# Optimization experiments

Measured on AMD Instinct MI355X. Metric: run time of the kernel, lower is better.

The kernel has to match this reference:

```python
import jax, jax.numpy as jnp
import numpy as np
import math


def get_alibi_slopes(n_heads: int) -> np.ndarray:
    # Bloom-style ALiBi slopes.
    cp2 = 2 ** math.floor(math.log2(n_heads))
    base = 2.0 ** (-(2.0 ** -(math.log2(cp2) - 3)))
    slopes = base ** np.arange(1, cp2 + 1, dtype=np.float32)
    if cp2 != n_heads:
        extra_base = 2.0 ** (-(2.0 ** -(math.log2(2 * cp2) - 3)))
        extra = extra_base ** np.arange(1, 2 * (n_heads - cp2) + 1, 2, dtype=np.float32)
        slopes = np.concatenate([slopes, extra])
    return slopes.astype(np.float32)


def setup_inputs() -> dict:
    key = jax.random.key(0)
    k1, k2, k3 = jax.random.split(key, 3)
    B, S, D, H = 2, 2048, 2048, 16
    T = B * S
    return {
        "hidden_states": jax.random.normal(k1, (T, D), dtype=jnp.float32) * 0.02,
        "qkv_weight": jax.random.normal(k2, (3, D, D), dtype=jnp.float32) * 0.02,
        "o_proj_weight": jax.random.normal(k3, (D, D), dtype=jnp.float32) * 0.02,
        "batch": B,
        "seq_len": S,
        "n_heads": H,
    }


def reference(hidden_states, qkv_weight, o_proj_weight, batch, seq_len, n_heads):
    T, D = hidden_states.shape
    head_dim = D // n_heads
    sm_scale = 1.0 / math.sqrt(head_dim)
    slopes = jnp.asarray(get_alibi_slopes(n_heads))  # [H]

    # QKV projection: equivalent of bmm(hidden.expand(3,-1,-1), qkv_weight)
    qkv = jnp.einsum("td,cde->cte", hidden_states, qkv_weight)  # [3, T, D]
    q, k, v = qkv.reshape(3, batch, seq_len, n_heads, head_dim)

    # Varlen causal attention with ALiBi (prefill / context phase).
    scores = jnp.einsum("bqhd,bkhd->bhqk", q, k) * sm_scale  # [B,H,S,S]
    pos = jnp.arange(seq_len)
    rel = (pos[None, :] - pos[:, None]).astype(jnp.float32)  # k_idx - q_idx
    scores = scores + slopes[None, :, None, None] * rel[None, None]
    causal = pos[None, :] <= pos[:, None]  # [S,S]
    scores = jnp.where(causal[None, None], scores, jnp.finfo(scores.dtype).min)
    probs = jax.nn.softmax(scores, axis=-1)
    attn = jnp.einsum("bhqk,bkhd->bqhd", probs, v)  # [B,S,H,Dh]

    attn = attn.reshape(T, D)
    return attn @ o_proj_weight
```

## Files before the change

kernel.cpp:

```cpp
#include <hip/hip_runtime.h>
#include <math.h>
#include <stdint.h>

typedef __bf16 bf16x8_t __attribute__((ext_vector_type(8)));
typedef float  f32x4_t  __attribute__((ext_vector_type(4)));
typedef unsigned short u16;


__device__ __forceinline__ u16 f2bf(float f) {
  unsigned u = __float_as_uint(f);
  u += 0x7FFFu + ((u >> 16) & 1u);
  return (u16)(u >> 16);
}

__device__ __forceinline__ void gload_lds16(const u16* gsrc, u16* ldst) {
  __builtin_amdgcn_global_load_lds(
      (__attribute__((address_space(1))) void*)(const_cast<u16*>(gsrc)),
      (__attribute__((address_space(3))) void*)(ldst),
      16, 0, 0);
}

__device__ __forceinline__ int sw8(int row, int e) { return e ^ ((row & 7) << 3); }

__device__ __forceinline__ void store_out(float* C, long idx, float v) { C[idx] = v; }
__device__ __forceinline__ void store_out(u16* C, long idx, float v) { C[idx] = f2bf(v); }

__device__ __forceinline__ float alibi_slope(int h, int H) {
  int cp2 = 1, lg = 0;
  while (cp2 * 2 <= H) { cp2 *= 2; lg++; }
  if (h < cp2) {
    double e = exp2((double)-(lg - 3));
    return (float)exp2(-e * (double)(h + 1));
  } else {
    double e = exp2((double)-(lg + 1 - 3));
    return (float)exp2(-e * (double)(2 * (h - cp2) + 1));
  }
}

#define FENCE() asm volatile("" ::: "memory")
#define BARRIER() do { FENCE(); __builtin_amdgcn_s_barrier(); \
                       __builtin_amdgcn_sched_barrier(0); FENCE(); } while (0)
#define WAITLGKM() do { asm volatile("s_waitcnt lgkmcnt(0)" ::: "memory"); \
                        __builtin_amdgcn_sched_barrier(0); } while (0)


__global__ __launch_bounds__(256) void k_cast_bf16(const float* __restrict__ in,
                                                   u16* __restrict__ out, long n) {
  long i = ((long)blockIdx.x * 256 + threadIdx.x) * 4;
  if (i + 3 < n) {
    float4 v = *reinterpret_cast<const float4*>(in + i);
    ushort4 o;
    o.x = f2bf(v.x); o.y = f2bf(v.y); o.z = f2bf(v.z); o.w = f2bf(v.w);
    *reinterpret_cast<ushort4*>(out + i) = o;
  }
}


__global__ __launch_bounds__(256) void k_transpose_cast(const float* __restrict__ in,
                                                        u16* __restrict__ out,
                                                        int R, int C) {
  __shared__ float tile[32][33];
  const float* inz = in + (long)blockIdx.z * R * C;
  u16* outz = out + (long)blockIdx.z * R * C;
  const int tx = threadIdx.x & 31, ty = threadIdx.x >> 5;
  const int r0 = blockIdx.y * 32, c0 = blockIdx.x * 32;
#pragma unroll
  for (int i = 0; i < 4; ++i)
    tile[ty + i * 8][tx] = inz[(long)(r0 + ty + i * 8) * C + c0 + tx];
  __syncthreads();
#pragma unroll
  for (int i = 0; i < 4; ++i)
    outz[(long)(c0 + ty + i * 8) * R + r0 + tx] = f2bf(tile[tx][ty + i * 8]);
}


__global__ __launch_bounds__(256) void k_transpose_v(const u16* __restrict__ V,
                                                     u16* __restrict__ Vt,
                                                     int S, int D, int Dh, int H) {
  __shared__ u16 tile[32][33];
  const int bh = blockIdx.z, b = bh / H, h = bh % H;
  const int tx = threadIdx.x & 31, ty = threadIdx.x >> 5;
  const int s0 = blockIdx.x * 32, d0 = blockIdx.y * 32;
  const u16* vin = V + (long)b * S * D + (long)h * Dh;
#pragma unroll
  for (int i = 0; i < 4; ++i)
    tile[ty + i * 8][tx] = vin[(long)(s0 + ty + i * 8) * D + d0 + tx];
  __syncthreads();
  u16* vout = Vt + (long)bh * Dh * S;
#pragma unroll
  for (int i = 0; i < 4; ++i)
    vout[(long)(d0 + ty + i * 8) * S + s0 + tx] = tile[tx][ty + i * 8];
}


__device__ __forceinline__ void stage16(const u16* __restrict__ g, long grow0, int K,
                                        int kt, int lr0, u16 (*lds)[64], int lane) {
  const int e = (lane & 7) * 8;
#pragma unroll
  for (int i = 0; i < 2; ++i) {
    const int r = lr0 + i * 8 + (lane >> 3);
    gload_lds16(g + (grow0 + r) * (long)K + kt + (e ^ ((r & 7) << 3)), &lds[lr0 + i * 8][0]);
  }
}

__device__ __forceinline__ void stage8(const u16* __restrict__ g, long grow0, int K,
                                       int kt, int lr0, u16 (*lds)[64], int lane) {
  const int e = (lane & 7) * 8;
  const int r = lr0 + (lane >> 3);
  gload_lds16(g + (grow0 + r) * (long)K + kt + (e ^ ((r & 7) << 3)), &lds[lr0][0]);
}


template <typename OUT_T>
__global__ __launch_bounds__(512, 2) void k_gemm8(const u16* __restrict__ A,
                                                  const u16* __restrict__ Bt,
                                                  OUT_T* __restrict__ Cb,
                                                  int M, int N, int K, long matStride,
                                                  float qs) {
  __shared__ u16 As[2][256][64];
  __shared__ u16 Bs[2][256][64];

  const int tid = threadIdx.x, wid = tid >> 6, lane = tid & 63;
  const int wr = wid >> 2, wc = wid & 3;
  const int frow = lane & 15, fk8 = (lane >> 4) * 8;
  const int orow = (lane >> 4) * 4, ocol = lane & 15;

  const int nwg = gridDim.x * gridDim.y;
  const int orig = blockIdx.y * gridDim.x + blockIdx.x;
  const int q = nwg >> 3, rr = nwg & 7;
  const int xcd = orig & 7, sl = orig >> 3;
  const int wg = (xcd < rr ? xcd * (q + 1) : rr * (q + 1) + (xcd - rr) * q) + sl;
  const int by = wg / gridDim.x, bx = wg % gridDim.x;

  const long abase = (long)by * 256, bbase = (long)bx * 256;

  const int bg0 = (wid >> 1) * 64 + (wid & 1) * 16;
  const int ag0 = (wid >> 2) * 128 + (wid & 3) * 16;

  f32x4_t acc[8][4];
#pragma unroll
  for (int m = 0; m < 8; ++m)
#pragma unroll
    for (int n = 0; n < 4; ++n)
#pragma unroll
      for (int r = 0; r < 4; ++r) acc[m][n][r] = 0.f;

  const int nt = K >> 6;

  stage16(Bt, bbase, K, 0, bg0, Bs[0], lane);
  stage16(Bt, bbase, K, 0, bg0 + 32, Bs[0], lane);
  stage16(A, abase, K, 0, ag0, As[0], lane);
  stage16(A, abase, K, 0, ag0 + 64, As[0], lane);
  asm volatile("s_waitcnt vmcnt(2)" ::: "memory");
  BARRIER();

  bf16x8_t afr[4][2], bfr[4][2];
  int cur = 0;

  for (int t = 0; t < nt; ++t) {
    const int ktn = (t + 1) << 6;
    const bool hn = (t + 1 < nt);
    const int nb = cur ^ 1;

#pragma unroll
    for (int m = 0; m < 4; ++m) {
      const int r = wr * 128 + m * 16 + frow;
      afr[m][0] = *reinterpret_cast<const bf16x8_t*>(&As[cur][r][sw8(r, fk8)]);
      afr[m][1] = *reinterpret_cast<const bf16x8_t*>(&As[cur][r][sw8(r, 32 + fk8)]);
    }
#pragma unroll
    for (int n = 0; n < 2; ++n) {
      const int r = wc * 64 + n * 16 + frow;
      bfr[n][0] = *reinterpret_cast<const bf16x8_t*>(&Bs[cur][r][sw8(r, fk8)]);
      bfr[n][1] = *reinterpret_cast<const bf16x8_t*>(&Bs[cur][r][sw8(r, 32 + fk8)]);
    }
    if (hn) stage16(Bt, bbase, K, ktn, bg0, Bs[nb], lane);
    BARRIER();
    WAITLGKM();
    __builtin_amdgcn_s_setprio(1);
#pragma unroll
    for (int m = 0; m < 4; ++m)
#pragma unroll
      for (int n = 0; n < 2; ++n) {
        acc[m][n] = __builtin_amdgcn_mfma_f32_16x16x32_bf16(afr[m][0], bfr[n][0], acc[m][n], 0, 0, 0);
        acc[m][n] = __builtin_amdgcn_mfma_f32_16x16x32_bf16(afr[m][1], bfr[n][1], acc[m][n], 0, 0, 0);
      }
    __builtin_amdgcn_s_setprio(0);
    BARRIER();

#pragma unroll
    for (int n = 0; n < 2; ++n) {
      const int r = wc * 64 + 32 + n * 16 + frow;
      bfr[2 + n][0] = *reinterpret_cast<const bf16x8_t*>(&Bs[cur][r][sw8(r, fk8)]);
      bfr[2 + n][1] = *reinterpret_cast<const bf16x8_t*>(&Bs[cur][r][sw8(r, 32 + fk8)]);
    }
    if (hn) stage16(Bt, bbase, K, ktn, bg0 + 32, Bs[nb], lane);
    BARRIER();
    WAITLGKM();
    __builtin_amdgcn_s_setprio(1);
#pragma unroll
    for (int m = 0; m < 4; ++m)
#pragma unroll
      for (int n = 0; n < 2; ++n) {
        acc[m][2 + n] = __builtin_amdgcn_mfma_f32_16x16x32_bf16(afr[m][0], bfr[2 + n][0], acc[m][2 + n], 0, 0, 0);
        acc[m][2 + n] = __builtin_amdgcn_mfma_f32_16x16x32_bf16(afr[m][1], bfr[2 + n][1], acc[m][2 + n], 0, 0, 0);
      }
    __builtin_amdgcn_s_setprio(0);
    if (hn) asm volatile("s_waitcnt vmcnt(4)" ::: "memory");
    else    asm volatile("s_waitcnt vmcnt(0)" ::: "memory");
    BARRIER();

#pragma unroll
    for (int m = 0; m < 4; ++m) {
      const int r = wr * 128 + 64 + m * 16 + frow;
      afr[m][0] = *reinterpret_cast<const bf16x8_t*>(&As[cur][r][sw8(r, fk8)]);
      afr[m][1] = *reinterpret_cast<const bf16x8_t*>(&As[cur][r][sw8(r, 32 + fk8)]);
    }
    if (hn) stage16(A, abase, K, ktn, ag0, As[nb], lane);
    BARRIER();
    WAITLGKM();
    __builtin_amdgcn_s_setprio(1);
#pragma unroll
    for (int m = 0; m < 4; ++m)
#pragma unroll
      for (int n = 0; n < 2; ++n) {
        acc[4 + m][n] = __builtin_amdgcn_mfma_f32_16x16x32_bf16(afr[m][0], bfr[n][0], acc[4 + m][n], 0, 0, 0);
        acc[4 + m][n] = __builtin_amdgcn_mfma_f32_16x16x32_bf16(afr[m][1], bfr[n][1], acc[4 + m][n], 0, 0, 0);
      }
    __builtin_amdgcn_s_setprio(0);
    BARRIER();

    if (hn) stage16(A, abase, K, ktn, ag0 + 64, As[nb], lane);
    __builtin_amdgcn_s_setprio(1);
#pragma unroll
    for (int m = 0; m < 4; ++m)
#pragma unroll
      for (int n = 0; n < 2; ++n) {
        acc[4 + m][2 + n] = __builtin_amdgcn_mfma_f32_16x16x32_bf16(afr[m][0], bfr[2 + n][0], acc[4 + m][2 + n], 0, 0, 0);
        acc[4 + m][2 + n] = __builtin_amdgcn_mfma_f32_16x16x32_bf16(afr[m][1], bfr[2 + n][1], acc[4 + m][2 + n], 0, 0, 0);
      }
    __builtin_amdgcn_s_setprio(0);
    if (hn) asm volatile("s_waitcnt vmcnt(2)" ::: "memory");
    BARRIER();

    cur ^= 1;
  }

#pragma unroll
  for (int m = 0; m < 8; ++m)
#pragma unroll
    for (int n = 0; n < 4; ++n)
#pragma unroll
      for (int r = 0; r < 4; ++r) {
        const long row = abase + wr * 128 + m * 16 + orow + r;
        const int col = (int)bbase + wc * 64 + n * 16 + ocol;
        const float sc = ((col >> 11) == 0) ? qs : 1.0f;
        const long idx = (long)(col >> 11) * matStride + row * 2048 + (col & 2047);
        store_out(Cb, idx, acc[m][n][r] * sc);
      }
}


template <typename OUT_T>
__global__ __launch_bounds__(512, 2) void k_gemm2(const u16* __restrict__ A,
                                                  const u16* __restrict__ Bt,
                                                  OUT_T* __restrict__ Cb,
                                                  int M, int N, int K, long matStride,
                                                  float qs) {
  __shared__ u16 As[2][128][64];
  __shared__ u16 Bs[2][256][64];

  const int tid = threadIdx.x, wid = tid >> 6, lane = tid & 63;
  const int wr = wid >> 2, wc = wid & 3;
  const int frow = lane & 15, fk8 = (lane >> 4) * 8;
  const int orow = (lane >> 4) * 4, ocol = lane & 15;

  const int nwg = gridDim.x * gridDim.y;
  const int orig = blockIdx.y * gridDim.x + blockIdx.x;
  const int q = nwg >> 3, rr = nwg & 7;
  const int xcd = orig & 7, sl = orig >> 3;
  const int wg = (xcd < rr ? xcd * (q + 1) : rr * (q + 1) + (xcd - rr) * q) + sl;
  const int by = wg / gridDim.x, bx = wg % gridDim.x;

  const long abase = (long)by * 128, bbase = (long)bx * 256;

  const int bg0 = (wid >> 1) * 64 + (wid & 1) * 16;
  const int ag0 = ((wid & 1) << 6) + ((wid >> 1) << 3);
  f32x4_t acc[4][4];
#pragma unroll
  for (int m = 0; m < 4; ++m)
#pragma unroll
    for (int n = 0; n < 4; ++n)
#pragma unroll
      for (int r = 0; r < 4; ++r) acc[m][n][r] = 0.f;

  const int nt = K >> 6;

  stage16(Bt, bbase, K, 0, bg0, Bs[0], lane);
  stage16(Bt, bbase, K, 0, bg0 + 32, Bs[0], lane);
  stage8 (A,  abase, K, 0, ag0, As[0], lane);
  stage8 (A,  abase, K, 0, ag0 + 32, As[0], lane);
  asm volatile("s_waitcnt vmcnt(1)" ::: "memory");
  BARRIER();

  bf16x8_t bfr[4][2], afr[2][2];
  int cur = 0;

  for (int t = 0; t < nt; ++t) {
    const int ktn = (t + 1) << 6;
    const bool hn = (t + 1 < nt);
    const int nb = cur ^ 1;

#pragma unroll
    for (int n = 0; n < 4; ++n) {
      const int r = wc * 64 + n * 16 + frow;
      bfr[n][0] = *reinterpret_cast<const bf16x8_t*>(&Bs[cur][r][sw8(r, fk8)]);
      bfr[n][1] = *reinterpret_cast<const bf16x8_t*>(&Bs[cur][r][sw8(r, 32 + fk8)]);
    }
#pragma unroll
    for (int m = 0; m < 2; ++m) {
      const int r = wr * 64 + m * 16 + frow;
      afr[m][0] = *reinterpret_cast<const bf16x8_t*>(&As[cur][r][sw8(r, fk8)]);
      afr[m][1] = *reinterpret_cast<const bf16x8_t*>(&As[cur][r][sw8(r, 32 + fk8)]);
    }
    if (hn) {
      stage16(Bt, bbase, K, ktn, bg0, Bs[nb], lane);
      stage16(Bt, bbase, K, ktn, bg0 + 32, Bs[nb], lane);
    }
    BARRIER();
    WAITLGKM();
    __builtin_amdgcn_s_setprio(1);
#pragma unroll
    for (int m = 0; m < 2; ++m)
#pragma unroll
      for (int n = 0; n < 4; ++n) {
        acc[m][n] = __builtin_amdgcn_mfma_f32_16x16x32_bf16(afr[m][0], bfr[n][0], acc[m][n], 0, 0, 0);
        acc[m][n] = __builtin_amdgcn_mfma_f32_16x16x32_bf16(afr[m][1], bfr[n][1], acc[m][n], 0, 0, 0);
      }
    __builtin_amdgcn_s_setprio(0);
    if (hn) asm volatile("s_waitcnt vmcnt(4)" ::: "memory");
    else    asm volatile("s_waitcnt vmcnt(0)" ::: "memory");
    BARRIER();

#pragma unroll
    for (int m = 0; m < 2; ++m) {
      const int r = wr * 64 + 32 + m * 16 + frow;
      afr[m][0] = *reinterpret_cast<const bf16x8_t*>(&As[cur][r][sw8(r, fk8)]);
      afr[m][1] = *reinterpret_cast<const bf16x8_t*>(&As[cur][r][sw8(r, 32 + fk8)]);
    }
    if (hn) {
      stage8(A, abase, K, ktn, ag0, As[nb], lane);
      stage8(A, abase, K, ktn, ag0 + 32, As[nb], lane);
    }
    BARRIER();
    WAITLGKM();
    __builtin_amdgcn_s_setprio(1);
#pragma unroll
    for (int m = 0; m < 2; ++m)
#pragma unroll
      for (int n = 0; n < 4; ++n) {
        acc[2 + m][n] = __builtin_amdgcn_mfma_f32_16x16x32_bf16(afr[m][0], bfr[n][0], acc[2 + m][n], 0, 0, 0);
        acc[2 + m][n] = __builtin_amdgcn_mfma_f32_16x16x32_bf16(afr[m][1], bfr[n][1], acc[2 + m][n], 0, 0, 0);
      }
    __builtin_amdgcn_s_setprio(0);
    if (hn) asm volatile("s_waitcnt vmcnt(1)" ::: "memory");
    BARRIER();

    cur ^= 1;
  }

#pragma unroll
  for (int m = 0; m < 4; ++m)
#pragma unroll
    for (int n = 0; n < 4; ++n)
#pragma unroll
      for (int r = 0; r < 4; ++r) {
        const long row = abase + wr * 64 + m * 16 + orow + r;
        const int col = (int)bbase + wc * 64 + n * 16 + ocol;
        const float sc = ((col >> 11) == 0) ? qs : 1.0f;
        const long idx = (long)(col >> 11) * matStride + row * 2048 + (col & 2047);
        store_out(Cb, idx, acc[m][n][r] * sc);
      }
}


__global__ __launch_bounds__(256) void k_attn(const u16* __restrict__ Q,
                                              const u16* __restrict__ Kb,
                                              const u16* __restrict__ Vt,
                                              u16* __restrict__ Out,
                                              int B, int S, int H, int D,
                                              float log2e) {
  __shared__ u16 Ks[64][128];
  __shared__ u16 Vs[128][64];
  __shared__ u16 Ps[64][64];

  const int tid = threadIdx.x, wid = tid >> 6, lane = tid & 63;

  const int nq = gridDim.x, nbh = gridDim.y;
  const int lin = blockIdx.x + nq * blockIdx.y;
  const int qb0 = lin / nbh;
  const int bh  = lin % nbh;
  const int qb  = (qb0 < nq / 2) ? qb0 : (nq + nq / 2 - 1 - qb0);

  const int b = bh / H, h = bh % H;
  const int Dh = D / H;

  const float slope2 = alibi_slope(h, H) * log2e;
  const long qrow0 = (long)b * S + qb * 64 + wid * 16;

  const int frow = lane & 15;
  const int fk8  = (lane >> 4) * 8;
  const int orow = (lane >> 4) * 4;
  const int ocol = lane & 15;

  bf16x8_t aq[4];
#pragma unroll
  for (int kk = 0; kk < 4; ++kk)
    aq[kk] = *reinterpret_cast<const bf16x8_t*>(
        Q + (qrow0 + frow) * (long)D + h * Dh + kk * 32 + fk8);

  float cw[4];
#pragma unroll
  for (int n = 0; n < 4; ++n) cw[n] = slope2 * (float)(n * 16 + ocol);

  f32x4_t oacc[8];
#pragma unroll
  for (int no = 0; no < 8; ++no)
#pragma unroll
    for (int r = 0; r < 4; ++r) oacc[no][r] = 0.f;

  float Mrun[4], lrun[4];
#pragma unroll
  for (int r = 0; r < 4; ++r) { Mrun[r] = -3.0e38f; lrun[r] = 0.f; }

  const u16* kbase = Kb + (long)b * S * D + h * Dh;
  const u16* vbase = Vt + (long)bh * Dh * S;

  const int ntile = qb + 1;

  for (int kt = 0; kt < ntile; ++kt) {
    __syncthreads();
#pragma unroll
    for (int i = 0; i < 4; ++i) {
      const int lr = i * 16 + wid * 4;
      const int r  = lr + (lane >> 4);
      gload_lds16(kbase + ((long)kt * 64 + r) * (long)D + sw8(r, (lane & 15) * 8), &Ks[lr][0]);
    }
#pragma unroll
    for (int i = 0; i < 4; ++i) {
      const int lr = i * 32 + wid * 8;
      const int r  = lr + (lane >> 3);
      gload_lds16(vbase + (long)r * S + kt * 64 + sw8(r, (lane & 7) * 8), &Vs[lr][0]);
    }
    __syncthreads();

    f32x4_t sacc[4];
#pragma unroll
    for (int n = 0; n < 4; ++n)
#pragma unroll
      for (int r = 0; r < 4; ++r) sacc[n][r] = 0.f;

#pragma unroll
    for (int kk = 0; kk < 4; ++kk) {
      bf16x8_t bk[4];
#pragma unroll
      for (int n = 0; n < 4; ++n) {
        const int krow = n * 16 + frow;
        bk[n] = *reinterpret_cast<const bf16x8_t*>(&Ks[krow][sw8(krow, kk * 32 + fk8)]);
      }
#pragma unroll
      for (int n = 0; n < 4; ++n)
        sacc[n] = __builtin_amdgcn_mfma_f32_16x16x32_bf16(aq[kk], bk[n], sacc[n], 0, 0, 0);
    }

    const float tb = slope2 * (float)(kt << 6);
    float cbn[4];
#pragma unroll
    for (int n = 0; n < 4; ++n) cbn[n] = tb + cw[n];

    float tmax[4];
#pragma unroll
    for (int r = 0; r < 4; ++r) tmax[r] = -3.0e38f;

    if (kt == qb) {
#pragma unroll
      for (int n = 0; n < 4; ++n)
#pragma unroll
        for (int r = 0; r < 4; ++r) {
          float v = sacc[n][r] + cbn[n];
          v = (n * 16 + ocol <= wid * 16 + orow + r) ? v : -1.0e30f;
          sacc[n][r] = v;
          tmax[r] = fmaxf(tmax[r], v);
        }
    } else {
#pragma unroll
      for (int n = 0; n < 4; ++n)
#pragma unroll
        for (int r = 0; r < 4; ++r) {
          const float v = sacc[n][r] + cbn[n];
          sacc[n][r] = v;
          tmax[r] = fmaxf(tmax[r], v);
        }
    }
#pragma unroll
    for (int r = 0; r < 4; ++r) {
      float t = tmax[r];
      t = fmaxf(t, __shfl_xor(t, 1));
      t = fmaxf(t, __shfl_xor(t, 2));
      t = fmaxf(t, __shfl_xor(t, 4));
      t = fmaxf(t, __shfl_xor(t, 8));
      tmax[r] = t;
    }

#pragma unroll
    for (int r = 0; r < 4; ++r) {
      const float mnew = fmaxf(Mrun[r], tmax[r]);
      const float alpha = exp2f(Mrun[r] - mnew);
      Mrun[r] = mnew;
      lrun[r] *= alpha;
#pragma unroll
      for (int no = 0; no < 8; ++no) oacc[no][r] *= alpha;
    }

    float tsum[4];
#pragma unroll
    for (int r = 0; r < 4; ++r) tsum[r] = 0.f;
#pragma unroll
    for (int n = 0; n < 4; ++n)
#pragma unroll
      for (int r = 0; r < 4; ++r) {
        const float p = exp2f(sacc[n][r] - Mrun[r]);
        tsum[r] += p;
        const int prow = wid * 16 + orow + r;
        Ps[prow][sw8(prow, n * 16 + ocol)] = f2bf(p);
      }
#pragma unroll
    for (int r = 0; r < 4; ++r) {
      float t = tsum[r];
      t += __shfl_xor(t, 1);
      t += __shfl_xor(t, 2);
      t += __shfl_xor(t, 4);
      t += __shfl_xor(t, 8);
      lrun[r] += t;
    }

    __syncthreads();

#pragma unroll
    for (int kk = 0; kk < 2; ++kk) {
      const int prow = wid * 16 + frow;
      bf16x8_t pa = *reinterpret_cast<const bf16x8_t*>(&Ps[prow][sw8(prow, kk * 32 + fk8)]);
#pragma unroll
      for (int no = 0; no < 8; ++no) {
        const int vrow = no * 16 + frow;
        bf16x8_t bv = *reinterpret_cast<const bf16x8_t*>(&Vs[vrow][sw8(vrow, kk * 32 + fk8)]);
        oacc[no] = __builtin_amdgcn_mfma_f32_16x16x32_bf16(pa, bv, oacc[no], 0, 0, 0);
      }
    }
  }

#pragma unroll
  for (int r = 0; r < 4; ++r) {
    const float rl = 1.0f / lrun[r];
    const long trow = qrow0 + orow + r;
#pragma unroll
    for (int no = 0; no < 8; ++no)
      Out[trow * (long)D + h * Dh + no * 16 + ocol] = f2bf(oacc[no][r] * rl);
  }
}


extern "C" void kernel_launch(void* const* d_in, const int* in_sizes, int n_in,
                              void* d_out, int out_size, void* d_ws, size_t ws_size,
                              hipStream_t stream) {
  const float* hs   = (const float*)d_in[0];
  const float* qkvw = (const float*)d_in[1];
  const float* ow   = (const float*)d_in[2];

  const int D = 2048, B = 2, H = 16;
  const long TD = (long)in_sizes[0];
  const long DD = (long)in_sizes[2];
  const int T = (int)(TD / D);
  const int S = T / B;
  const int Dh = D / H;
  const float log2e = 1.44269504f;
  const float qs = (1.0f / sqrtf((float)Dh)) * log2e;

  u16* ws  = (u16*)d_ws;
  u16* hsb = ws;
  u16* wt  = ws + TD;
  u16* owt = wt + 3 * DD;
  u16* qkv = owt + DD;
  u16* vt   = wt;
  u16* attn = hsb;

  k_cast_bf16<<<dim3((unsigned)(TD / 1024)), 256, 0, stream>>>(hs, hsb, TD);
  k_transpose_cast<<<dim3(D / 32, D / 32, 3), 256, 0, stream>>>(qkvw, wt, D, D);
  k_transpose_cast<<<dim3(D / 32, D / 32, 1), 256, 0, stream>>>(ow, owt, D, D);
  k_gemm8<u16><<<dim3((3 * D) / 256, T / 256), 512, 0, stream>>>(
      hsb, wt, qkv, T, 3 * D, D, TD, qs);
  k_transpose_v<<<dim3(S / 32, Dh / 32, B * H), 256, 0, stream>>>(
      qkv + 2 * TD, vt, S, D, Dh, H);
  k_attn<<<dim3(S / 64, B * H), 256, 0, stream>>>(
      qkv, qkv + TD, vt, attn, B, S, H, D, log2e);
  k_gemm2<float><<<dim3(D / 256, T / 128), 512, 0, stream>>>(
      attn, owt, (float*)d_out, T, D, D, 0L, 1.0f);
}
```

Baseline: 292.4 us.

## Shrink QKV GEMM K-tile to 32 and raise occupancy to four blocks per CU

```diff
diff --git a/kernel.cpp b/kernel.cpp
--- a/kernel.cpp
+++ b/kernel.cpp
@@ -21,6 +21,7 @@
 }
 
 __device__ __forceinline__ int sw8(int row, int e) { return e ^ ((row & 7) << 3); }
+__device__ __forceinline__ int sw32(int row, int e) { return e ^ (((row >> 1) & 3) << 3); }
 
 __device__ __forceinline__ void store_out(float* C, long idx, float v) { C[idx] = v; }
 __device__ __forceinline__ void store_out(u16* C, long idx, float v) { C[idx] = f2bf(v); }
@@ -110,15 +111,22 @@
   gload_lds16(g + (grow0 + r) * (long)K + kt + (e ^ ((r & 7) << 3)), &lds[lr0][0]);
 }
 
+__device__ __forceinline__ void stage32(const u16* __restrict__ g, long grow0, int K,
+                                        int kt, int lr0, u16 (*lds)[32], int lane) {
+  const int r = lr0 + (lane >> 2);
+  const int e = (lane & 3) * 8;
+  gload_lds16(g + (grow0 + r) * (long)K + kt + sw32(r, e), &lds[lr0][0]);
+}
+
 
 template <typename OUT_T>
-__global__ __launch_bounds__(512, 2) void k_gemm8(const u16* __restrict__ A,
-                                                  const u16* __restrict__ Bt,
-                                                  OUT_T* __restrict__ Cb,
-                                                  int M, int N, int K, long matStride,
-                                                  float qs) {
-  __shared__ u16 As[2][256][64];
-  __shared__ u16 Bs[2][256][64];
+__global__ __launch_bounds__(512, 4) void k_gemm32(const u16* __restrict__ A,
+                                                   const u16* __restrict__ Bt,
+                                                   OUT_T* __restrict__ Cb,
+                                                   int M, int N, int K, long matStride,
+                                                   float qs) {
+  __shared__ u16 As[2][256][32];
+  __shared__ u16 Bs[2][256][32];
 
   const int tid = threadIdx.x, wid = tid >> 6, lane = tid & 63;
   const int wr = wid >> 2, wc = wid & 3;
@@ -134,8 +142,7 @@
 
   const long abase = (long)by * 256, bbase = (long)bx * 256;
 
-  const int bg0 = (wid >> 1) * 64 + (wid & 1) * 16;
-  const int ag0 = (wid >> 2) * 128 + (wid & 3) * 16;
+  const int sg0 = wid * 32;
 
   f32x4_t acc[8][4];
 #pragma unroll
@@ -145,102 +152,92 @@
 #pragma unroll
       for (int r = 0; r < 4; ++r) acc[m][n][r] = 0.f;
 
-  const int nt = K >> 6;
-
-  stage16(Bt, bbase, K, 0, bg0, Bs[0], lane);
-  stage16(Bt, bbase, K, 0, bg0 + 32, Bs[0], lane);
-  stage16(A, abase, K, 0, ag0, As[0], lane);
-  stage16(A, abase, K, 0, ag0 + 64, As[0], lane);
-  asm volatile("s_waitcnt vmcnt(2)" ::: "memory");
+  const int nt = K >> 5;
+
+  stage32(Bt, bbase, K, 0, sg0, Bs[0], lane);
+  stage32(Bt, bbase, K, 0, sg0 + 16, Bs[0], lane);
+  stage32(A, abase, K, 0, sg0, As[0], lane);
+  stage32(A, abase, K, 0, sg0 + 16, As[0], lane);
+  asm volatile("s_waitcnt vmcnt(0)" ::: "memory");
   BARRIER();
 
-  bf16x8_t afr[4][2], bfr[4][2];
+  bf16x8_t a0[4], a1[4], b0[2], b1[2];
   int cur = 0;
 
   for (int t = 0; t < nt; ++t) {
-    const int ktn = (t + 1) << 6;
+    const int ktn = (t + 1) << 5;
     const bool hn = (t + 1 < nt);
     const int nb = cur ^ 1;
 
 #pragma unroll
     for (int m = 0; m < 4; ++m) {
       const int r = wr * 128 + m * 16 + frow;
-      afr[m][0] = *reinterpret_cast<const bf16x8_t*>(&As[cur][r][sw8(r, fk8)]);
-      afr[m][1] = *reinterpret_cast<const bf16x8_t*>(&As[cur][r][sw8(r, 32 + fk8)]);
+      a0[m] = *reinterpret_cast<const bf16x8_t*>(&As[cur][r][sw32(r, fk8)]);
     }
 #pragma unroll
     for (int n = 0; n < 2; ++n) {
       const int r = wc * 64 + n * 16 + frow;
-      bfr[n][0] = *reinterpret_cast<const bf16x8_t*>(&Bs[cur][r][sw8(r, fk8)]);
-      bfr[n][1] = *reinterpret_cast<const bf16x8_t*>(&Bs[cur][r][sw8(r, 32 + fk8)]);
-    }
-    if (hn) stage16(Bt, bbase, K, ktn, bg0, Bs[nb], lane);
+      b0[n] = *reinterpret_cast<const bf16x8_t*>(&Bs[cur][r][sw32(r, fk8)]);
+    }
+    if (hn) {
+      stage32(Bt, bbase, K, ktn, sg0, Bs[nb], lane);
+      stage32(Bt, bbase, K, ktn, sg0 + 16, Bs[nb], lane);
+    }
     BARRIER();
     WAITLGKM();
     __builtin_amdgcn_s_setprio(1);
 #pragma unroll
     for (int m = 0; m < 4; ++m)
 #pragma unroll
-      for (int n = 0; n < 2; ++n) {
-        acc[m][n] = __builtin_amdgcn_mfma_f32_16x16x32_bf16(afr[m][0], bfr[n][0], acc[m][n], 0, 0, 0);
-        acc[m][n] = __builtin_amdgcn_mfma_f32_16x16x32_bf16(afr[m][1], bfr[n][1], acc[m][n], 0, 0, 0);
-      }
+      for (int n = 0; n < 2; ++n)
+        acc[m][n] = __builtin_amdgcn_mfma_f32_16x16x32_bf16(a0[m], b0[n], acc[m][n], 0, 0, 0);
     __builtin_amdgcn_s_setprio(0);
     BARRIER();
 
 #pragma unroll
     for (int n = 0; n < 2; ++n) {
       const int r = wc * 64 + 32 + n * 16 + frow;
-      bfr[2 + n][0] = *reinterpret_cast<const bf16x8_t*>(&Bs[cur][r][sw8(r, fk8)]);
-      bfr[2 + n][1] = *reinterpret_cast<const bf16x8_t*>(&Bs[cur][r][sw8(r, 32 + fk8)]);
-    }
-    if (hn) stage16(Bt, bbase, K, ktn, bg0 + 32, Bs[nb], lane);
+      b1[n] = *reinterpret_cast<const bf16x8_t*>(&Bs[cur][r][sw32(r, fk8)]);
+    }
+    if (hn) {
+      stage32(A, abase, K, ktn, sg0, As[nb], lane);
+      stage32(A, abase, K, ktn, sg0 + 16, As[nb], lane);
+    }
     BARRIER();
     WAITLGKM();
     __builtin_amdgcn_s_setprio(1);
 #pragma unroll
     for (int m = 0; m < 4; ++m)
 #pragma unroll
-      for (int n = 0; n < 2; ++n) {
-        acc[m][2 + n] = __builtin_amdgcn_mfma_f32_16x16x32_bf16(afr[m][0], bfr[2 + n][0], acc[m][2 + n], 0, 0, 0);
-        acc[m][2 + n] = __builtin_amdgcn_mfma_f32_16x16x32_bf16(afr[m][1], bfr[2 + n][1], acc[m][2 + n], 0, 0, 0);
-      }
+      for (int n = 0; n < 2; ++n)
+        acc[m][2 + n] = __builtin_amdgcn_mfma_f32_16x16x32_bf16(a0[m], b1[n], acc[m][2 + n], 0, 0, 0);
     __builtin_amdgcn_s_setprio(0);
-    if (hn) asm volatile("s_waitcnt vmcnt(4)" ::: "memory");
-    else    asm volatile("s_waitcnt vmcnt(0)" ::: "memory");
     BARRIER();
 
 #pragma unroll
     for (int m = 0; m < 4; ++m) {
       const int r = wr * 128 + 64 + m * 16 + frow;
-      afr[m][0] = *reinterpret_cast<const bf16x8_t*>(&As[cur][r][sw8(r, fk8)]);
-      afr[m][1] = *reinterpret_cast<const bf16x8_t*>(&As[cur][r][sw8(r, 32 + fk8)]);
-    }
-    if (hn) stage16(A, abase, K, ktn, ag0, As[nb], lane);
+      a1[m] = *reinterpret_cast<const bf16x8_t*>(&As[cur][r][sw32(r, fk8)]);
+    }
     BARRIER();
     WAITLGKM();
     __builtin_amdgcn_s_setprio(1);
 #pragma unroll
     for (int m = 0; m < 4; ++m)
 #pragma unroll
-      for (int n = 0; n < 2; ++n) {
-        acc[4 + m][n] = __builtin_amdgcn_mfma_f32_16x16x32_bf16(afr[m][0], bfr[n][0], acc[4 + m][n], 0, 0, 0);
-        acc[4 + m][n] = __builtin_amdgcn_mfma_f32_16x16x32_bf16(afr[m][1], bfr[n][1], acc[4 + m][n], 0, 0, 0);
-      }
+      for (int n = 0; n < 2; ++n)
+        acc[4 + m][n] = __builtin_amdgcn_mfma_f32_16x16x32_bf16(a1[m], b0[n], acc[4 + m][n], 0, 0, 0);
     __builtin_amdgcn_s_setprio(0);
     BARRIER();
 
-    if (hn) stage16(A, abase, K, ktn, ag0 + 64, As[nb], lane);
     __builtin_amdgcn_s_setprio(1);
 #pragma unroll
     for (int m = 0; m < 4; ++m)
 #pragma unroll
-      for (int n = 0; n < 2; ++n) {
-        acc[4 + m][2 + n] = __builtin_amdgcn_mfma_f32_16x16x32_bf16(afr[m][0], bfr[2 + n][0], acc[4 + m][2 + n], 0, 0, 0);
-        acc[4 + m][2 + n] = __builtin_amdgcn_mfma_f32_16x16x32_bf16(afr[m][1], bfr[2 + n][1], acc[4 + m][2 + n], 0, 0, 0);
-      }
+      for (int n = 0; n < 2; ++n)
+        acc[4 + m][2 + n] = __builtin_amdgcn_mfma_f32_16x16x32_bf16(a1[m], b1[n], acc[4 + m][2 + n], 0, 0, 0);
     __builtin_amdgcn_s_setprio(0);
-    if (hn) asm volatile("s_waitcnt vmcnt(2)" ::: "memory");
+    if (hn) asm volatile("s_waitcnt vmcnt(0)" ::: "memory");
     BARRIER();
 
     cur ^= 1;
@@ -286,6 +283,7 @@
 
   const int bg0 = (wid >> 1) * 64 + (wid & 1) * 16;
   const int ag0 = ((wid & 1) << 6) + ((wid >> 1) << 3);
+
   f32x4_t acc[4][4];
 #pragma unroll
   for (int m = 0; m < 4; ++m)
@@ -597,7 +595,7 @@
   k_cast_bf16<<<dim3((unsigned)(TD / 1024)), 256, 0, stream>>>(hs, hsb, TD);
   k_transpose_cast<<<dim3(D / 32, D / 32, 3), 256, 0, stream>>>(qkvw, wt, D, D);
   k_transpose_cast<<<dim3(D / 32, D / 32, 1), 256, 0, stream>>>(ow, owt, D, D);
-  k_gemm8<u16><<<dim3((3 * D) / 256, T / 256), 512, 0, stream>>>(
+  k_gemm32<u16><<<dim3((3 * D) / 256, T / 256), 512, 0, stream>>>(
       hsb, wt, qkv, T, 3 * D, D, TD, qs);
   k_transpose_v<<<dim3(S / 32, Dh / 32, B * H), 256, 0, stream>>>(
       qkv + 2 * TD, vt, S, D, Dh, H);
```

Measured after the change: 988.1 us (median of 2 runs). +237.9%, slower.

## Widen QKV GEMM tile to 256x384 with single-buffered A in LDS

Applied to the files above, without the earlier changes.

```diff
diff --git a/kernel.cpp b/kernel.cpp
--- a/kernel.cpp
+++ b/kernel.cpp
@@ -112,13 +112,13 @@
 
 
 template <typename OUT_T>
-__global__ __launch_bounds__(512, 2) void k_gemm8(const u16* __restrict__ A,
-                                                  const u16* __restrict__ Bt,
-                                                  OUT_T* __restrict__ Cb,
-                                                  int M, int N, int K, long matStride,
-                                                  float qs) {
-  __shared__ u16 As[2][256][64];
-  __shared__ u16 Bs[2][256][64];
+__global__ __launch_bounds__(512, 2) void k_gemm384(const u16* __restrict__ A,
+                                                    const u16* __restrict__ Bt,
+                                                    OUT_T* __restrict__ Cb,
+                                                    int M, int N, int K, long matStride,
+                                                    float qs) {
+  __shared__ u16 As[256][64];
+  __shared__ u16 Bs[2][384][64];
 
   const int tid = threadIdx.x, wid = tid >> 6, lane = tid & 63;
   const int wr = wid >> 2, wc = wid & 3;
@@ -132,29 +132,30 @@
   const int wg = (xcd < rr ? xcd * (q + 1) : rr * (q + 1) + (xcd - rr) * q) + sl;
   const int by = wg / gridDim.x, bx = wg % gridDim.x;
 
-  const long abase = (long)by * 256, bbase = (long)bx * 256;
-
-  const int bg0 = (wid >> 1) * 64 + (wid & 1) * 16;
-  const int ag0 = (wid >> 2) * 128 + (wid & 3) * 16;
-
-  f32x4_t acc[8][4];
+  const long abase = (long)by * 256, bbase = (long)bx * 384;
+
+  const int bg0 = wid * 48;
+  const int ag0 = wid * 32;
+
+  f32x4_t acc[8][6];
 #pragma unroll
   for (int m = 0; m < 8; ++m)
 #pragma unroll
-    for (int n = 0; n < 4; ++n)
+    for (int n = 0; n < 6; ++n)
 #pragma unroll
       for (int r = 0; r < 4; ++r) acc[m][n][r] = 0.f;
 
   const int nt = K >> 6;
 
   stage16(Bt, bbase, K, 0, bg0, Bs[0], lane);
+  stage16(Bt, bbase, K, 0, bg0 + 16, Bs[0], lane);
   stage16(Bt, bbase, K, 0, bg0 + 32, Bs[0], lane);
-  stage16(A, abase, K, 0, ag0, As[0], lane);
-  stage16(A, abase, K, 0, ag0 + 64, As[0], lane);
-  asm volatile("s_waitcnt vmcnt(2)" ::: "memory");
+  stage16(A, abase, K, 0, ag0, As, lane);
+  stage16(A, abase, K, 0, ag0 + 16, As, lane);
+  asm volatile("s_waitcnt vmcnt(0)" ::: "memory");
   BARRIER();
 
-  bf16x8_t afr[4][2], bfr[4][2];
+  bf16x8_t afr[4][2], bfr[6][2];
   int cur = 0;
 
   for (int t = 0; t < nt; ++t) {
@@ -165,12 +166,12 @@
 #pragma unroll
     for (int m = 0; m < 4; ++m) {
       const int r = wr * 128 + m * 16 + frow;
-      afr[m][0] = *reinterpret_cast<const bf16x8_t*>(&As[cur][r][sw8(r, fk8)]);
-      afr[m][1] = *reinterpret_cast<const bf16x8_t*>(&As[cur][r][sw8(r, 32 + fk8)]);
+      afr[m][0] = *reinterpret_cast<const bf16x8_t*>(&As[r][sw8(r, fk8)]);
+      afr[m][1] = *reinterpret_cast<const bf16x8_t*>(&As[r][sw8(r, 32 + fk8)]);
     }
 #pragma unroll
     for (int n = 0; n < 2; ++n) {
-      const int r = wc * 64 + n * 16 + frow;
+      const int r = wc * 96 + n * 16 + frow;
       bfr[n][0] = *reinterpret_cast<const bf16x8_t*>(&Bs[cur][r][sw8(r, fk8)]);
       bfr[n][1] = *reinterpret_cast<const bf16x8_t*>(&Bs[cur][r][sw8(r, 32 + fk8)]);
     }
@@ -189,10 +190,30 @@
     BARRIER();
 
 #pragma unroll
-    for (int n = 0; n < 2; ++n) {
-      const int r = wc * 64 + 32 + n * 16 + frow;
-      bfr[2 + n][0] = *reinterpret_cast<const bf16x8_t*>(&Bs[cur][r][sw8(r, fk8)]);
-      bfr[2 + n][1] = *reinterpret_cast<const bf16x8_t*>(&Bs[cur][r][sw8(r, 32 + fk8)]);
+    for (int n = 2; n < 4; ++n) {
+      const int r = wc * 96 + n * 16 + frow;
+      bfr[n][0] = *reinterpret_cast<const bf16x8_t*>(&Bs[cur][r][sw8(r, fk8)]);
+      bfr[n][1] = *reinterpret_cast<const bf16x8_t*>(&Bs[cur][r][sw8(r, 32 + fk8)]);
+    }
+    if (hn) stage16(Bt, bbase, K, ktn, bg0 + 16, Bs[nb], lane);
+    BARRIER();
+    WAITLGKM();
+    __builtin_amdgcn_s_setprio(1);
+#pragma unroll
+    for (int m = 0; m < 4; ++m)
+#pragma unroll
+      for (int n = 2; n < 4; ++n) {
+        acc[m][n] = __builtin_amdgcn_mfma_f32_16x16x32_bf16(afr[m][0], bfr[n][0], acc[m][n], 0, 0, 0);
+        acc[m][n] = __builtin_amdgcn_mfma_f32_16x16x32_bf16(afr[m][1], bfr[n][1], acc[m][n], 0, 0, 0);
+      }
+    __builtin_amdgcn_s_setprio(0);
+    BARRIER();
+
+#pragma unroll
+    for (int n = 4; n < 6; ++n) {
+      const int r = wc * 96 + n * 16 + frow;
+      bfr[n][0] = *reinterpret_cast<const bf16x8_t*>(&Bs[cur][r][sw8(r, fk8)]);
+      bfr[n][1] = *reinterpret_cast<const bf16x8_t*>(&Bs[cur][r][sw8(r, 32 + fk8)]);
     }
     if (hn) stage16(Bt, bbase, K, ktn, bg0 + 32, Bs[nb], lane);
     BARRIER();
@@ -201,22 +222,19 @@
 #pragma unroll
     for (int m = 0; m < 4; ++m)
 #pragma unroll
-      for (int n = 0; n < 2; ++n) {
-        acc[m][2 + n] = __builtin_amdgcn_mfma_f32_16x16x32_bf16(afr[m][0], bfr[2 + n][0], acc[m][2 + n], 0, 0, 0);
-        acc[m][2 + n] = __builtin_amdgcn_mfma_f32_16x16x32_bf16(afr[m][1], bfr[2 + n][1], acc[m][2 + n], 0, 0, 0);
-      }
-    __builtin_amdgcn_s_setprio(0);
-    if (hn) asm volatile("s_waitcnt vmcnt(4)" ::: "memory");
-    else    asm volatile("s_waitcnt vmcnt(0)" ::: "memory");
+      for (int n = 4; n < 6; ++n) {
+        acc[m][n] = __builtin_amdgcn_mfma_f32_16x16x32_bf16(afr[m][0], bfr[n][0], acc[m][n], 0, 0, 0);
+        acc[m][n] = __builtin_amdgcn_mfma_f32_16x16x32_bf16(afr[m][1], bfr[n][1], acc[m][n], 0, 0, 0);
+      }
+    __builtin_amdgcn_s_setprio(0);
     BARRIER();
 
 #pragma unroll
     for (int m = 0; m < 4; ++m) {
       const int r = wr * 128 + 64 + m * 16 + frow;
-      afr[m][0] = *reinterpret_cast<const bf16x8_t*>(&As[cur][r][sw8(r, fk8)]);
-      afr[m][1] = *reinterpret_cast<const bf16x8_t*>(&As[cur][r][sw8(r, 32 + fk8)]);
-    }
-    if (hn) stage16(A, abase, K, ktn, ag0, As[nb], lane);
+      afr[m][0] = *reinterpret_cast<const bf16x8_t*>(&As[r][sw8(r, fk8)]);
+      afr[m][1] = *reinterpret_cast<const bf16x8_t*>(&As[r][sw8(r, 32 + fk8)]);
+    }
     BARRIER();
     WAITLGKM();
     __builtin_amdgcn_s_setprio(1);
@@ -230,17 +248,31 @@
     __builtin_amdgcn_s_setprio(0);
     BARRIER();
 
-    if (hn) stage16(A, abase, K, ktn, ag0 + 64, As[nb], lane);
+    if (hn) {
+      stage16(A, abase, K, ktn, ag0, As, lane);
+      stage16(A, abase, K, ktn, ag0 + 16, As, lane);
+    }
     __builtin_amdgcn_s_setprio(1);
 #pragma unroll
     for (int m = 0; m < 4; ++m)
 #pragma unroll
-      for (int n = 0; n < 2; ++n) {
-        acc[4 + m][2 + n] = __builtin_amdgcn_mfma_f32_16x16x32_bf16(afr[m][0], bfr[2 + n][0], acc[4 + m][2 + n], 0, 0, 0);
-        acc[4 + m][2 + n] = __builtin_amdgcn_mfma_f32_16x16x32_bf16(afr[m][1], bfr[2 + n][1], acc[4 + m][2 + n], 0, 0, 0);
-      }
-    __builtin_amdgcn_s_setprio(0);
-    if (hn) asm volatile("s_waitcnt vmcnt(2)" ::: "memory");
+      for (int n = 2; n < 4; ++n) {
+        acc[4 + m][n] = __builtin_amdgcn_mfma_f32_16x16x32_bf16(afr[m][0], bfr[n][0], acc[4 + m][n], 0, 0, 0);
+        acc[4 + m][n] = __builtin_amdgcn_mfma_f32_16x16x32_bf16(afr[m][1], bfr[n][1], acc[4 + m][n], 0, 0, 0);
+      }
+    __builtin_amdgcn_s_setprio(0);
+    BARRIER();
+
+    __builtin_amdgcn_s_setprio(1);
+#pragma unroll
+    for (int m = 0; m < 4; ++m)
+#pragma unroll
+      for (int n = 4; n < 6; ++n) {
+        acc[4 + m][n] = __builtin_amdgcn_mfma_f32_16x16x32_bf16(afr[m][0], bfr[n][0], acc[4 + m][n], 0, 0, 0);
+        acc[4 + m][n] = __builtin_amdgcn_mfma_f32_16x16x32_bf16(afr[m][1], bfr[n][1], acc[4 + m][n], 0, 0, 0);
+      }
+    __builtin_amdgcn_s_setprio(0);
+    if (hn) asm volatile("s_waitcnt vmcnt(0)" ::: "memory");
     BARRIER();
 
     cur ^= 1;
@@ -249,11 +281,11 @@
 #pragma unroll
   for (int m = 0; m < 8; ++m)
 #pragma unroll
-    for (int n = 0; n < 4; ++n)
+    for (int n = 0; n < 6; ++n)
 #pragma unroll
       for (int r = 0; r < 4; ++r) {
         const long row = abase + wr * 128 + m * 16 + orow + r;
-        const int col = (int)bbase + wc * 64 + n * 16 + ocol;
+        const int col = (int)bbase + wc * 96 + n * 16 + ocol;
         const float sc = ((col >> 11) == 0) ? qs : 1.0f;
         const long idx = (long)(col >> 11) * matStride + row * 2048 + (col & 2047);
         store_out(Cb, idx, acc[m][n][r] * sc);
@@ -286,6 +318,7 @@
 
   const int bg0 = (wid >> 1) * 64 + (wid & 1) * 16;
   const int ag0 = ((wid & 1) << 6) + ((wid >> 1) << 3);
+
   f32x4_t acc[4][4];
 #pragma unroll
   for (int m = 0; m < 4; ++m)
@@ -597,7 +630,7 @@
   k_cast_bf16<<<dim3((unsigned)(TD / 1024)), 256, 0, stream>>>(hs, hsb, TD);
   k_transpose_cast<<<dim3(D / 32, D / 32, 3), 256, 0, stream>>>(qkvw, wt, D, D);
   k_transpose_cast<<<dim3(D / 32, D / 32, 1), 256, 0, stream>>>(ow, owt, D, D);
-  k_gemm8<u16><<<dim3((3 * D) / 256, T / 256), 512, 0, stream>>>(
+  k_gemm384<u16><<<dim3((3 * D) / 384, T / 256), 512, 0, stream>>>(
       hsb, wt, qkv, T, 3 * D, D, TD, qs);
   k_transpose_v<<<dim3(S / 32, Dh / 32, B * H), 256, 0, stream>>>(
       qkv + 2 * TD, vt, S, D, Dh, H);
```

After: 466.0 us. 1.59x slower.
